# Kernel tuning notes

Measured on AMD Instinct MI355X. Metric: run time of the kernel, lower is better.

## Reference

```python
import jax, jax.numpy as jnp
import numpy as np

DIM = 768
NUM_HEADS = 12
HEAD_DIM = DIM // NUM_HEADS
SCALE = HEAD_DIM ** -0.5


def setup_inputs() -> dict:
    key = jax.random.key(0)
    k1, k2, k3, k4, k5 = jax.random.split(key, 5)
    B, N = 2, 2048
    x = jax.random.normal(k1, (B, N, DIM), dtype=jnp.float32)
    # nn.Linear weights stored as [out, in]; we keep them as [in, out] for jnp use.
    Wq = jax.random.normal(k2, (DIM, DIM), dtype=jnp.float32) * (DIM ** -0.5)
    Wkv = jax.random.normal(k3, (DIM, 2 * HEAD_DIM), dtype=jnp.float32) * (DIM ** -0.5)
    Wproj = jax.random.normal(k4, (DIM, DIM), dtype=jnp.float32) * (DIM ** -0.5)
    bproj = jax.random.normal(k5, (DIM,), dtype=jnp.float32) * 0.01
    return {"x": x, "Wq": Wq, "Wkv": Wkv, "Wproj": Wproj, "bproj": bproj, "num_layer": 0}


def reference(x, Wq, Wkv, Wproj, bproj, num_layer):
    B, N, C = x.shape
    H, D = NUM_HEADS, HEAD_DIM
    q = (x @ Wq).reshape(B, N, H, D).transpose(0, 2, 1, 3)        # [B,H,N,D]
    kv = (x @ Wkv).reshape(B, N, 2, D)
    k, v = kv[:, :, 0, :], kv[:, :, 1, :]                          # [B,N,D] shared across heads (MQA)
    attn = jnp.einsum('bhid,bjd->bhij', q, k) * SCALE              # [B,H,N,N]
    attn = jax.nn.softmax(attn, axis=-1)
    out = jnp.einsum('bhij,bjd->bhid', attn, v)                    # [B,H,N,D]
    out = out.transpose(0, 2, 1, 3).reshape(B, N, C)
    return out @ Wproj + bproj
```

## Files before the change

kernel.cpp:

```cpp
#include <hip/hip_runtime.h>

#define BATCH 2
#define SEQ   2048
#define DIMC  768
#define HEADS 12
#define HD    64
#define QSCALE 0.1803368801111204f

typedef short bf16x8 __attribute__((ext_vector_type(8)));
typedef float f32x16 __attribute__((ext_vector_type(16)));

__device__ __forceinline__ unsigned short f2bf(float f) {
    union { float f; unsigned int u; } a; a.f = f;
    unsigned int r = a.u + 0x7fffu + ((a.u >> 16) & 1u);
    return (unsigned short)(r >> 16);
}
__device__ __forceinline__ unsigned int pack2bf(float lo, float hi) {
    union { float f; unsigned int u; } a, b; a.f = lo; b.f = hi;
    return __builtin_amdgcn_perm(b.u + 0x8000u, a.u + 0x8000u, 0x07060302);
}
__device__ __forceinline__ float exp2f_fast(float x) { return __builtin_amdgcn_exp2f(x); }

__global__ void prep(const float* __restrict__ Wq, const float* __restrict__ Wkv,
                     const float* __restrict__ Wproj, unsigned short* __restrict__ WqT,
                     unsigned short* __restrict__ WkvT, unsigned short* __restrict__ WprT)
{
    const int bid = blockIdx.x, t = threadIdx.x;
    __shared__ float sT[32][33];
    const float* W; unsigned short* WT; int N, tb;
    if (bid < 576)      { W = Wq;    WT = WqT;  N = DIMC;   tb = bid; }
    else if (bid < 672) { W = Wkv;   WT = WkvT; N = 2 * HD; tb = bid - 576; }
    else                { W = Wproj; WT = WprT; N = DIMC;   tb = bid - 672; }
    const int tilesN = N / 32;
    const int k0 = (tb / tilesN) * 32, n0 = (tb - (tb / tilesN) * tilesN) * 32;
    const int r = t >> 3, c4 = (t & 7) * 4;
    float4 v = *(const float4*)&W[(size_t)(k0 + r) * N + n0 + c4];
    sT[c4 + 0][r] = v.x; sT[c4 + 1][r] = v.y; sT[c4 + 2][r] = v.z; sT[c4 + 3][r] = v.w;
    __syncthreads();
    ushort4 o = { f2bf(sT[r][c4]), f2bf(sT[r][c4 + 1]), f2bf(sT[r][c4 + 2]), f2bf(sT[r][c4 + 3]) };
    *(ushort4*)&WT[(size_t)(n0 + r) * 768 + k0 + c4] = o;
}

template <int MODE>
__global__ __launch_bounds__(256)
void gemm64(const void* __restrict__ Asrc, const unsigned short* __restrict__ BT,
            const float* __restrict__ bias, void* __restrict__ C0,
            unsigned short* __restrict__ Kout, unsigned short* __restrict__ VTout)
{
    __shared__ __align__(16) unsigned short sA[2][64][40];
    __shared__ __align__(16) unsigned short sB[2][64][40];
    const int t = threadIdx.x, lane = t & 63, w = t >> 6;
    const int l31 = lane & 31, hi = lane >> 5;
    const int mh = w >> 1, nh = w & 1;
    const int bm = blockIdx.y * 64, bn = blockIdx.x * 64;

    const int ar = t >> 2, ac = (t & 3) * 8;
    const float* Af = (const float*)Asrc;
    const unsigned short* Ab = (const unsigned short*)Asrc;
    const unsigned short* Bp = &BT[(size_t)(bn + ar) * 768 + ac];

    float4 xa0, xa1; bf16x8 aab; bf16x8 bb;
    auto loadT = [&](int ki) {
        if (MODE == 0) {
            const float* p = &Af[(size_t)(bm + ar) * 768 + ki * 32 + ac];
            xa0 = *(const float4*)p; xa1 = *(const float4*)(p + 4);
        } else {
            aab = *(const bf16x8*)&Ab[(size_t)(bm + ar) * 768 + ki * 32 + ac];
        }
        bb = *(const bf16x8*)&Bp[ki * 32];
    };
    auto writeT = [&](int bf) {
        if (MODE == 0) {
            uint4 o = { pack2bf(xa0.x, xa0.y), pack2bf(xa0.z, xa0.w),
                        pack2bf(xa1.x, xa1.y), pack2bf(xa1.z, xa1.w) };
            *(uint4*)&sA[bf][ar][ac] = o;
        } else {
            *(bf16x8*)&sA[bf][ar][ac] = aab;
        }
        *(bf16x8*)&sB[bf][ar][ac] = bb;
    };

    loadT(0); writeT(0); loadT(1);
    __syncthreads();

    f32x16 acc = {};
    for (int ki = 0; ki < 24; ++ki) {
        const int buf = ki & 1;
        if (ki + 1 < 24) {
            writeT(buf ^ 1);
            loadT(ki + 2 < 24 ? ki + 2 : 23);
        }
        #pragma unroll
        for (int s = 0; s < 2; ++s) {
            bf16x8 a = *(const bf16x8*)&sA[buf][mh * 32 + l31][s * 16 + hi * 8];
            bf16x8 b = *(const bf16x8*)&sB[buf][nh * 32 + l31][s * 16 + hi * 8];
            acc = __builtin_amdgcn_mfma_f32_32x32x16_bf16(a, b, acc, 0, 0, 0);
        }
        __syncthreads();
    }

    const int n = bn + nh * 32 + l31;
    #pragma unroll
    for (int r = 0; r < 16; ++r) {
        const int m = bm + mh * 32 + (r & 3) + 8 * (r >> 2) + 4 * hi;
        float val = acc[r];
        if (MODE == 0) {
            if (n < 768) {
                ((unsigned short*)C0)[(size_t)m * 768 + n] = f2bf(val * QSCALE);
            } else {
                int c2 = n - 768;
                if (c2 < HD) Kout[(size_t)m * HD + c2] = f2bf(val);
                else {
                    int bbk = m >> 11, tok = m & (SEQ - 1);
                    VTout[(size_t)bbk * HD * SEQ + (size_t)(c2 - HD) * SEQ + tok] = f2bf(val);
                }
            }
        } else {
            ((float*)C0)[(size_t)m * 768 + n] = val + bias[n];
        }
    }
}

__global__ __launch_bounds__(256)
void flash_kernel(const unsigned short* __restrict__ Qw, const unsigned short* __restrict__ Kw,
                  const unsigned short* __restrict__ VTw, unsigned short* __restrict__ Ob)
{
    const int qblk = blockIdx.x, h = blockIdx.y, b = blockIdx.z;
    const int tid = threadIdx.x, w = tid >> 6, lane = tid & 63;
    const int l31 = lane & 31, hi = lane >> 5;
    const int kr = w >> 1, qc = w & 1;

    __shared__ __align__(16) unsigned short sK [2][64][72];
    __shared__ __align__(16) unsigned short sVT[2][64][72];
    __shared__ float sL[4][32];
    __shared__ float sLi[2][32];

    const size_t qrow = (size_t)(b * SEQ + qblk * 64 + qc * 32 + l31);
    bf16x8 qf[4];
    #pragma unroll
    for (int s = 0; s < 4; ++s)
        qf[s] = *(const bf16x8*)&Qw[qrow * DIMC + h * HD + s * 16 + hi * 8];

    f32x16 oacc0 = {}, oacc1 = {};
    float lsum = 0.0f;

    const int r_st = tid >> 2, c_st = (tid & 3) * 16;
    const unsigned short* Kp  = &Kw[(size_t)(b * SEQ + r_st) * HD + c_st];
    const unsigned short* VTp = &VTw[(size_t)b * HD * SEQ + (size_t)r_st * SEQ + c_st];

    bf16x8 kg0, kg1, vg0, vg1;
    auto loadKV = [&](int ti) {
        const unsigned short* ks = Kp + (size_t)ti * 64 * HD;
        const unsigned short* vs = VTp + ti * 64;
        kg0 = *(const bf16x8*)&ks[0]; kg1 = *(const bf16x8*)&ks[8];
        vg0 = *(const bf16x8*)&vs[0]; vg1 = *(const bf16x8*)&vs[8];
    };
    auto writeKV = [&](int bf) {
        *(bf16x8*)&sK[bf][r_st][c_st]      = kg0;
        *(bf16x8*)&sK[bf][r_st][c_st + 8]  = kg1;
        *(bf16x8*)&sVT[bf][r_st][c_st]     = vg0;
        *(bf16x8*)&sVT[bf][r_st][c_st + 8] = vg1;
    };

    loadKV(0); writeKV(0); loadKV(1);
    __syncthreads();

    for (int kt = 0; kt < SEQ / 64; ++kt) {
        const int buf = kt & 1;
        if (kt + 1 < SEQ / 64) {
            writeKV(buf ^ 1);
            loadKV(kt + 2 < SEQ / 64 ? kt + 2 : SEQ / 64 - 1);
        }

        f32x16 st = {};
        #pragma unroll
        for (int s = 0; s < 4; ++s) {
            bf16x8 ka = *(const bf16x8*)&sK[buf][kr * 32 + l31][s * 16 + hi * 8];
            st = __builtin_amdgcn_mfma_f32_32x32x16_bf16(ka, qf[s], st, 0, 0, 0);
        }

        uint2 pg[4];
        #pragma unroll
        for (int g = 0; g < 4; ++g) {
            float p0 = exp2f_fast(st[g * 4 + 0]);
            float p1 = exp2f_fast(st[g * 4 + 1]);
            float p2 = exp2f_fast(st[g * 4 + 2]);
            float p3 = exp2f_fast(st[g * 4 + 3]);
            lsum += (p0 + p1) + (p2 + p3);
            pg[g].x = pack2bf(p0, p1);
            pg[g].y = pack2bf(p2, p3);
        }

        #pragma unroll
        for (int s = 0; s < 2; ++s) {
            uint2 send; send.x = hi ? pg[2 * s].x : pg[2 * s + 1].x;
                        send.y = hi ? pg[2 * s].y : pg[2 * s + 1].y;
            uint2 recv; recv.x = __shfl_xor((int)send.x, 32);
                        recv.y = __shfl_xor((int)send.y, 32);
            union { uint4 u4; bf16x8 v; } pa;
            pa.u4.x = hi ? recv.x : pg[2 * s].x;
            pa.u4.y = hi ? recv.y : pg[2 * s].y;
            pa.u4.z = hi ? pg[2 * s + 1].x : recv.x;
            pa.u4.w = hi ? pg[2 * s + 1].y : recv.y;
            bf16x8 vb0 = *(const bf16x8*)&sVT[buf][l31][kr * 32 + s * 16 + hi * 8];
            bf16x8 vb1 = *(const bf16x8*)&sVT[buf][32 + l31][kr * 32 + s * 16 + hi * 8];
            oacc0 = __builtin_amdgcn_mfma_f32_32x32x16_bf16(pa.v, vb0, oacc0, 0, 0, 0);
            oacc1 = __builtin_amdgcn_mfma_f32_32x32x16_bf16(pa.v, vb1, oacc1, 0, 0, 0);
        }
        __syncthreads();
    }

    lsum += __shfl_xor(lsum, 32);
    if (lane < 32) sL[w][l31] = lsum;

    float* scratch = (float*)&sK[0][0][0];
    {
        int rid = qc * 2 + (1 - kr);
        float* rg = scratch + rid * 1024;
        f32x16 give = kr ? oacc0 : oacc1;
        #pragma unroll
        for (int r = 0; r < 16; ++r) rg[r * 64 + lane] = give[r];
    }
    __syncthreads();

    f32x16 own = kr ? oacc1 : oacc0;
    {
        const float* rg = scratch + (qc * 2 + kr) * 1024;
        #pragma unroll
        for (int r = 0; r < 16; ++r) own[r] += rg[r * 64 + lane];
    }
    if (kr == 0 && lane < 32)
        sLi[qc][l31] = 1.0f / (sL[qc][l31] + sL[qc + 2][l31]);
    __syncthreads();

    #pragma unroll
    for (int r = 0; r < 16; ++r) {
        int rq = (r & 3) + 8 * (r >> 2) + 4 * hi;
        float iv = sLi[qc][rq];
        size_t row = (size_t)(b * SEQ + qblk * 64 + qc * 32 + rq);
        Ob[row * DIMC + h * HD + kr * 32 + l31] = f2bf(own[r] * iv);
    }
}

extern "C" void kernel_launch(void* const* d_in, const int* in_sizes, int n_in,
                              void* d_out, int out_size, void* d_ws, size_t ws_size,
                              hipStream_t stream)
{
    const float* x     = (const float*)d_in[0];
    const float* Wq    = (const float*)d_in[1];
    const float* Wkv   = (const float*)d_in[2];
    const float* Wproj = (const float*)d_in[3];
    const float* bproj = (const float*)d_in[4];

    const int M = BATCH * SEQ;
    unsigned short* WqT  = (unsigned short*)d_ws;
    unsigned short* WkvT = WqT  + DIMC * DIMC;
    unsigned short* WprT = WkvT + 2 * HD * DIMC;
    unsigned short* Qw   = WprT + DIMC * DIMC;
    unsigned short* Kw   = Qw   + (size_t)M * DIMC;
    unsigned short* VTw  = Kw   + (size_t)M * HD;
    unsigned short* Ob   = VTw  + (size_t)BATCH * HD * SEQ;

    prep<<<1248, 256, 0, stream>>>(Wq, Wkv, Wproj, WqT, WkvT, WprT);
    gemm64<0><<<dim3(14, M / 64), 256, 0, stream>>>(x, WqT, nullptr, Qw, Kw, VTw);
    flash_kernel<<<dim3(SEQ / 64, HEADS, BATCH), 256, 0, stream>>>(Qw, Kw, VTw, Ob);
    gemm64<1><<<dim3(12, M / 64), 256, 0, stream>>>(Ob, WprT, bproj, d_out, nullptr, nullptr);
}
```

Measured before the change: 153.2 us.

## Use 128x128 GEMM tiles with direct global-to-LDS loads and prepacked bf16 input

Replaces the 64x64 projection GEMM with a 128x128 tile kernel where each wave computes a 64x64 sub-tile from 16 MFMA 16x16x32 accumulators. Operand tiles are streamed into LDS with global_load_lds, bypassing registers. The fp32 input x is converted to bf16 in the prep kernel, staged in the buffer later reused for the attention output. The aim is more operand reuse per LDS byte and fewer load instructions, at the cost of fewer blocks (fewer CUs busy), unpadded LDS rows that may bank-conflict, and an extra pass over x.

Measured after the change: 168.1 us. 1.1x slower.

```diff
diff --git a/kernel.cpp b/kernel.cpp
--- a/kernel.cpp
+++ b/kernel.cpp
@@ -8,6 +8,7 @@
 #define QSCALE 0.1803368801111204f
 
 typedef short bf16x8 __attribute__((ext_vector_type(8)));
+typedef float f32x4  __attribute__((ext_vector_type(4)));
 typedef float f32x16 __attribute__((ext_vector_type(16)));
 
 __device__ __forceinline__ unsigned short f2bf(float f) {
@@ -21,11 +22,27 @@
 }
 __device__ __forceinline__ float exp2f_fast(float x) { return __builtin_amdgcn_exp2f(x); }
 
+__device__ __forceinline__ void gload16(const unsigned short* g, unsigned short* l) {
+    __builtin_amdgcn_global_load_lds(
+        (const __attribute__((address_space(1))) unsigned int*)g,
+        (__attribute__((address_space(3))) unsigned int*)l, 16, 0, 0);
+}
+
 __global__ void prep(const float* __restrict__ Wq, const float* __restrict__ Wkv,
-                     const float* __restrict__ Wproj, unsigned short* __restrict__ WqT,
-                     unsigned short* __restrict__ WkvT, unsigned short* __restrict__ WprT)
+                     const float* __restrict__ Wproj, const float* __restrict__ x,
+                     unsigned short* __restrict__ WqT, unsigned short* __restrict__ WkvT,
+                     unsigned short* __restrict__ WprT, unsigned short* __restrict__ xb)
 {
     const int bid = blockIdx.x, t = threadIdx.x;
+    if (bid >= 1248) {
+        const size_t base = (size_t)(bid - 1248) * 2048 + (size_t)t * 8;
+        float4 v0 = *(const float4*)&x[base];
+        float4 v1 = *(const float4*)&x[base + 4];
+        uint4 o = { pack2bf(v0.x, v0.y), pack2bf(v0.z, v0.w),
+                    pack2bf(v1.x, v1.y), pack2bf(v1.z, v1.w) };
+        *(uint4*)&xb[base] = o;
+        return;
+    }
     __shared__ float sT[32][33];
     const float* W; unsigned short* WT; int N, tb;
     if (bid < 576)      { W = Wq;    WT = WqT;  N = DIMC;   tb = bid; }
@@ -43,80 +60,80 @@
 
 template <int MODE>
 __global__ __launch_bounds__(256)
-void gemm64(const void* __restrict__ Asrc, const unsigned short* __restrict__ BT,
-            const float* __restrict__ bias, void* __restrict__ C0,
-            unsigned short* __restrict__ Kout, unsigned short* __restrict__ VTout)
-{
-    __shared__ __align__(16) unsigned short sA[2][64][40];
-    __shared__ __align__(16) unsigned short sB[2][64][40];
+void gemm128(const unsigned short* __restrict__ A, const unsigned short* __restrict__ BT,
+             const float* __restrict__ bias, void* __restrict__ C0,
+             unsigned short* __restrict__ Kout, unsigned short* __restrict__ VTout)
+{
+    __shared__ __align__(16) unsigned short sA[2][128 * 32];
+    __shared__ __align__(16) unsigned short sB[2][128 * 32];
     const int t = threadIdx.x, lane = t & 63, w = t >> 6;
-    const int l31 = lane & 31, hi = lane >> 5;
-    const int mh = w >> 1, nh = w & 1;
-    const int bm = blockIdx.y * 64, bn = blockIdx.x * 64;
-
-    const int ar = t >> 2, ac = (t & 3) * 8;
-    const float* Af = (const float*)Asrc;
-    const unsigned short* Ab = (const unsigned short*)Asrc;
-    const unsigned short* Bp = &BT[(size_t)(bn + ar) * 768 + ac];
-
-    float4 xa0, xa1; bf16x8 aab; bf16x8 bb;
-    auto loadT = [&](int ki) {
-        if (MODE == 0) {
-            const float* p = &Af[(size_t)(bm + ar) * 768 + ki * 32 + ac];
-            xa0 = *(const float4*)p; xa1 = *(const float4*)(p + 4);
-        } else {
-            aab = *(const bf16x8*)&Ab[(size_t)(bm + ar) * 768 + ki * 32 + ac];
-        }
-        bb = *(const bf16x8*)&Bp[ki * 32];
+    const int bm = blockIdx.y * 128, bn = blockIdx.x * 128;
+    const int wm = (w >> 1) * 64, wn = (w & 1) * 64;
+
+    const int cr = lane >> 2, ck = (lane & 3) * 8;
+    const int row0 = w * 32 + cr, row1 = row0 + 16;
+    const unsigned short* Ap0 = &A [(size_t)(bm + row0) * DIMC + ck];
+    const unsigned short* Ap1 = &A [(size_t)(bm + row1) * DIMC + ck];
+    const unsigned short* Bp0 = &BT[(size_t)(bn + row0) * DIMC + ck];
+    const unsigned short* Bp1 = &BT[(size_t)(bn + row1) * DIMC + ck];
+
+    auto stage = [&](int kt, int bf) {
+        const int off = kt * 32;
+        gload16(Ap0 + off, &sA[bf][(w * 2) * 512]);
+        gload16(Ap1 + off, &sA[bf][(w * 2) * 512 + 512]);
+        gload16(Bp0 + off, &sB[bf][(w * 2) * 512]);
+        gload16(Bp1 + off, &sB[bf][(w * 2) * 512 + 512]);
     };
-    auto writeT = [&](int bf) {
-        if (MODE == 0) {
-            uint4 o = { pack2bf(xa0.x, xa0.y), pack2bf(xa0.z, xa0.w),
-                        pack2bf(xa1.x, xa1.y), pack2bf(xa1.z, xa1.w) };
-            *(uint4*)&sA[bf][ar][ac] = o;
-        } else {
-            *(bf16x8*)&sA[bf][ar][ac] = aab;
-        }
-        *(bf16x8*)&sB[bf][ar][ac] = bb;
-    };
-
-    loadT(0); writeT(0); loadT(1);
-    __syncthreads();
-
-    f32x16 acc = {};
-    for (int ki = 0; ki < 24; ++ki) {
-        const int buf = ki & 1;
-        if (ki + 1 < 24) {
-            writeT(buf ^ 1);
-            loadT(ki + 2 < 24 ? ki + 2 : 23);
-        }
-        #pragma unroll
-        for (int s = 0; s < 2; ++s) {
-            bf16x8 a = *(const bf16x8*)&sA[buf][mh * 32 + l31][s * 16 + hi * 8];
-            bf16x8 b = *(const bf16x8*)&sB[buf][nh * 32 + l31][s * 16 + hi * 8];
-            acc = __builtin_amdgcn_mfma_f32_32x32x16_bf16(a, b, acc, 0, 0, 0);
-        }
+
+    const int fr = lane & 15, fk = (lane >> 4) * 8;
+
+    f32x4 acc[4][4] = {};
+
+    stage(0, 0);
+    __syncthreads();
+    for (int kt = 0; kt < DIMC / 32; ++kt) {
+        const int buf = kt & 1;
+        if (kt + 1 < DIMC / 32) stage(kt + 1, buf ^ 1);
+        bf16x8 af[4], bq[4];
+        #pragma unroll
+        for (int i = 0; i < 4; ++i)
+            af[i] = *(const bf16x8*)&sA[buf][(wm + i * 16 + fr) * 32 + fk];
+        #pragma unroll
+        for (int j = 0; j < 4; ++j)
+            bq[j] = *(const bf16x8*)&sB[buf][(wn + j * 16 + fr) * 32 + fk];
+        #pragma unroll
+        for (int i = 0; i < 4; ++i)
+            #pragma unroll
+            for (int j = 0; j < 4; ++j)
+                acc[i][j] = __builtin_amdgcn_mfma_f32_16x16x32_bf16(af[i], bq[j], acc[i][j], 0, 0, 0);
         __syncthreads();
     }
 
-    const int n = bn + nh * 32 + l31;
+    const int cn = lane & 15, cm = (lane >> 4) * 4;
     #pragma unroll
-    for (int r = 0; r < 16; ++r) {
-        const int m = bm + mh * 32 + (r & 3) + 8 * (r >> 2) + 4 * hi;
-        float val = acc[r];
-        if (MODE == 0) {
-            if (n < 768) {
-                ((unsigned short*)C0)[(size_t)m * 768 + n] = f2bf(val * QSCALE);
-            } else {
-                int c2 = n - 768;
-                if (c2 < HD) Kout[(size_t)m * HD + c2] = f2bf(val);
-                else {
-                    int bbk = m >> 11, tok = m & (SEQ - 1);
-                    VTout[(size_t)bbk * HD * SEQ + (size_t)(c2 - HD) * SEQ + tok] = f2bf(val);
+    for (int j = 0; j < 4; ++j) {
+        const int n = bn + wn + j * 16 + cn;
+        #pragma unroll
+        for (int i = 0; i < 4; ++i) {
+            #pragma unroll
+            for (int r = 0; r < 4; ++r) {
+                const int m = bm + wm + i * 16 + cm + r;
+                float val = acc[i][j][r];
+                if (MODE == 0) {
+                    if (n < DIMC) {
+                        ((unsigned short*)C0)[(size_t)m * DIMC + n] = f2bf(val * QSCALE);
+                    } else {
+                        const int c2 = n - DIMC;
+                        if (c2 < HD) Kout[(size_t)m * HD + c2] = f2bf(val);
+                        else {
+                            const int bbk = m >> 11, tok = m & (SEQ - 1);
+                            VTout[(size_t)bbk * HD * SEQ + (size_t)(c2 - HD) * SEQ + tok] = f2bf(val);
+                        }
+                    }
+                } else {
+                    ((float*)C0)[(size_t)m * DIMC + n] = val + bias[n];
                 }
             }
-        } else {
-            ((float*)C0)[(size_t)m * 768 + n] = val + bias[n];
         }
     }
 }
@@ -260,9 +277,10 @@
     unsigned short* Kw   = Qw   + (size_t)M * DIMC;
     unsigned short* VTw  = Kw   + (size_t)M * HD;
     unsigned short* Ob   = VTw  + (size_t)BATCH * HD * SEQ;
-
-    prep<<<1248, 256, 0, stream>>>(Wq, Wkv, Wproj, WqT, WkvT, WprT);
-    gemm64<0><<<dim3(14, M / 64), 256, 0, stream>>>(x, WqT, nullptr, Qw, Kw, VTw);
+    unsigned short* xb   = Ob;
+
+    prep<<<1248 + 1536, 256, 0, stream>>>(Wq, Wkv, Wproj, x, WqT, WkvT, WprT, xb);
+    gemm128<0><<<dim3(7, M / 128), 256, 0, stream>>>(xb, WqT, nullptr, Qw, Kw, VTw);
     flash_kernel<<<dim3(SEQ / 64, HEADS, BATCH), 256, 0, stream>>>(Qw, Kw, VTw, Ob);
-    gemm64<1><<<dim3(12, M / 64), 256, 0, stream>>>(Ob, WprT, bproj, d_out, nullptr, nullptr);
-}
+    gemm128<1><<<dim3(6, M / 128), 256, 0, stream>>>(Ob, WprT, bproj, d_out, nullptr, nullptr);
+}
```
